# Optimization experiments

Hardware: AMD Instinct MI355X
Metric: run time of the kernel (lower is better)

The kernel has to match this reference:

```python
import jax, jax.numpy as jnp
import numpy as np

EPS = 1e-7
N = 100000
E = 1600000
IN_DIM = 128
OUT_DIM = 128


def _norm(t):
    # clamped L2 norm over last dim, keepdims
    return jnp.clip(jnp.linalg.norm(t, axis=-1, keepdims=True), EPS, None)


def log_map_zero(x, c):
    sqrt_c = jnp.sqrt(c)
    xn = _norm(x)
    y = jnp.clip(sqrt_c * xn, None, 1.0 - 1e-5)
    return jnp.arctanh(y) * x / (sqrt_c * xn)


def exp_map_zero(v, c):
    sqrt_c = jnp.sqrt(c)
    vn = _norm(v)
    return jnp.tanh(sqrt_c * vn) * v / (sqrt_c * vn)


def setup_inputs() -> dict:
    key = jax.random.key(0)
    k1, k2, k3, k4 = jax.random.split(key, 4)
    x = 0.1 * jax.random.normal(k1, (N, IN_DIM), dtype=jnp.float32)  # inside ball
    edge_index = jax.random.randint(k2, (2, E), 0, N, dtype=jnp.int64)
    c = jnp.ones((), dtype=jnp.float32)
    # Xavier-uniform weight (out_dim, in_dim)
    limit = float(np.sqrt(6.0 / (IN_DIM + OUT_DIM)))
    weight = jax.random.uniform(k3, (OUT_DIM, IN_DIM), minval=-limit, maxval=limit, dtype=jnp.float32)
    bias = jnp.zeros((OUT_DIM,), dtype=jnp.float32)
    return {"x": x, "edge_index": edge_index, "c": c, "num_nodes": N,
            "weight": weight, "bias": bias}


def reference(x, edge_index, c, num_nodes, weight, bias):
    # 1. log-map all node features to tangent space at origin
    v = log_map_zero(x, c)  # (N, in_dim)
    src, dst = edge_index[0], edge_index[1]
    # 2. mean aggregation over neighbours (incl. self) via segment_sum
    agg = jax.ops.segment_sum(v[src], dst, num_segments=num_nodes) + v
    count = jax.ops.segment_sum(jnp.ones((src.shape[0],), dtype=v.dtype), dst,
                                num_segments=num_nodes) + 1.0
    v_agg = agg / jnp.clip(count, 1.0, None)[:, None]
    # 3. back to hyperbolic space, then hyperbolic linear
    x_hyp = exp_map_zero(v_agg, c)
    v2 = log_map_zero(x_hyp, c)
    out = v2 @ weight.T + bias
    return exp_map_zero(out, c)
```

## Files before the change

### kernel.cpp

```cpp
#include <hip/hip_runtime.h>
#include <math.h>

#define EPSF 1e-7f
#define YMAXF 0.99999f
#define WPITCH 136

#define NBUCK 256
#define PB_CHUNK 2048

typedef short bf16x8 __attribute__((ext_vector_type(8)));
typedef short bf16x4 __attribute__((ext_vector_type(4)));
typedef float f32x4  __attribute__((ext_vector_type(4)));
typedef int   i32x4  __attribute__((ext_vector_type(4)));

__device__ __forceinline__ float grp32_sum(float v) {
    v += __shfl_xor(v, 1);
    v += __shfl_xor(v, 2);
    v += __shfl_xor(v, 4);
    v += __shfl_xor(v, 8);
    v += __shfl_xor(v, 16);
    return v;
}

__device__ __forceinline__ short f2bf(float f) {
    unsigned u = __float_as_uint(f);
    unsigned r = (u + 0x7FFFu + ((u >> 16) & 1u)) >> 16;
    return (short)r;
}

__device__ __forceinline__ float bf2f(short u) {
    return __uint_as_float(((unsigned)(unsigned short)u) << 16);
}

__device__ __forceinline__ float bf_lo(int w) {
    return __uint_as_float(((unsigned)w) << 16);
}
__device__ __forceinline__ float bf_hi(int w) {
    return __uint_as_float(((unsigned)w) & 0xffff0000u);
}

__global__ void logmap_kernel(const float* __restrict__ x,
                              const float* __restrict__ c_ptr,
                              short* __restrict__ v_bf,
                              int N) {
    int gid = blockIdx.x * blockDim.x + threadIdx.x;
    int row = gid >> 5;
    if (row >= N) return;
    int lane = gid & 31;
    const float4 xv = ((const float4*)x)[(size_t)row * 32 + lane];
    float ss = xv.x * xv.x + xv.y * xv.y + xv.z * xv.z + xv.w * xv.w;
    ss = grp32_sum(ss);
    float sc = sqrtf(c_ptr[0]);
    float xn = fmaxf(sqrtf(ss), EPSF);
    float y = fminf(sc * xn, YMAXF);
    float s = atanhf(y) / (sc * xn);
    bf16x4 pk;
    pk[0] = f2bf(s * xv.x); pk[1] = f2bf(s * xv.y);
    pk[2] = f2bf(s * xv.z); pk[3] = f2bf(s * xv.w);
    *(bf16x4*)&v_bf[(size_t)row * 128 + lane * 4] = pk;
}

__global__ __launch_bounds__(256)
void bucket_count_kernel(const int* __restrict__ eidx_dst,
                         int* __restrict__ bucketCount, int E) {
    __shared__ int h[NBUCK];
    int tid = threadIdx.x;
    h[tid] = 0;
    __syncthreads();
    int per = (E + gridDim.x - 1) / gridDim.x;
    int start = blockIdx.x * per;
    int end = min(start + per, E);
    for (int i = start + tid; i < end; i += 256)
        atomicAdd(&h[eidx_dst[i] >> 9], 1);
    __syncthreads();
    if (h[tid]) atomicAdd(&bucketCount[tid], h[tid]);
}

__global__ __launch_bounds__(256)
void bucket_scan_kernel(const int* __restrict__ bucketCount,
                        int* __restrict__ bucket_base,
                        int* __restrict__ cursor) {
    __shared__ int part[256];
    int tid = threadIdx.x;
    int val = bucketCount[tid];
    part[tid] = val;
    __syncthreads();
    for (int off = 1; off < 256; off <<= 1) {
        int t = (tid >= off) ? part[tid - off] : 0;
        __syncthreads();
        part[tid] += t;
        __syncthreads();
    }
    int excl = part[tid] - val;
    bucket_base[tid] = excl;
    cursor[tid] = excl;
}

__global__ __launch_bounds__(256)
void bucket_scatter_kernel(const int* __restrict__ eidx,
                           int* __restrict__ cursor,
                           int* __restrict__ bucketed, int E) {
    __shared__ int hist[NBUCK];
    __shared__ int lstart[NBUCK];
    __shared__ int gbase[NBUCK];
    __shared__ int part[256];
    __shared__ int stage[PB_CHUNK];
    __shared__ unsigned char stageB[PB_CHUNK];

    int tid = threadIdx.x;
    int start = blockIdx.x * PB_CHUNK;
    int cnt = min(PB_CHUNK, E - start);
    hist[tid] = 0;
    __syncthreads();

    const int J = PB_CHUNK / 256;
    int myP[J], myB[J], myR[J];
    #pragma unroll
    for (int j = 0; j < J; ++j) {
        int idx = j * 256 + tid;
        myR[j] = -1;
        if (idx < cnt) {
            int e = start + idx;
            int d = eidx[E + e];
            int s = eidx[e];
            int b = d >> 9;
            myB[j] = b;
            myP[j] = ((d & 511) << 17) | s;
            myR[j] = atomicAdd(&hist[b], 1);
        }
    }
    __syncthreads();
    part[tid] = hist[tid];
    __syncthreads();
    for (int off = 1; off < 256; off <<= 1) {
        int t = (tid >= off) ? part[tid - off] : 0;
        __syncthreads();
        part[tid] += t;
        __syncthreads();
    }
    lstart[tid] = part[tid] - hist[tid];
    if (hist[tid]) gbase[tid] = atomicAdd(&cursor[tid], hist[tid]);
    __syncthreads();
    #pragma unroll
    for (int j = 0; j < J; ++j) {
        if (myR[j] >= 0) {
            int pos = lstart[myB[j]] + myR[j];
            stage[pos] = myP[j];
            stageB[pos] = (unsigned char)myB[j];
        }
    }
    __syncthreads();
    for (int i = tid; i < cnt; i += 256) {
        int b = stageB[i];
        bucketed[gbase[b] + (i - lstart[b])] = stage[i];
    }
}

__global__ __launch_bounds__(256)
void csr_kernel(const int* __restrict__ bucketed,
                const int* __restrict__ bucket_base,
                const int* __restrict__ cursor_post,
                int* __restrict__ offsets, int* __restrict__ deg,
                int* __restrict__ sorted_src, int N) {
    __shared__ int hist[512];
    __shared__ int pre[512];
    __shared__ int cur[512];
    __shared__ int part[256];
    int b = blockIdx.x;
    int tid = threadIdx.x;
    int start = bucket_base[b];
    int end = cursor_post[b];
    hist[tid] = 0;
    hist[tid + 256] = 0;
    __syncthreads();
    for (int i = start + tid; i < end; i += 256)
        atomicAdd(&hist[bucketed[i] >> 17], 1);
    __syncthreads();
    int a0 = hist[2 * tid], a1 = hist[2 * tid + 1];
    part[tid] = a0 + a1;
    __syncthreads();
    for (int off = 1; off < 256; off <<= 1) {
        int t = (tid >= off) ? part[tid - off] : 0;
        __syncthreads();
        part[tid] += t;
        __syncthreads();
    }
    int base2 = part[tid] - (a0 + a1);
    pre[2 * tid] = base2;
    pre[2 * tid + 1] = base2 + a0;
    cur[2 * tid] = base2;
    cur[2 * tid + 1] = base2 + a0;
    __syncthreads();
    int node0 = b << 9;
    for (int i = tid; i < 512; i += 256) {
        int node = node0 + i;
        if (node < N) { offsets[node] = start + pre[i]; deg[node] = hist[i]; }
    }
    for (int i = start + tid; i < end; i += 256) {
        int p = bucketed[i];
        int ld = p >> 17;
        int src = p & 0x1FFFF;
        int r = atomicAdd(&cur[ld], 1);
        sorted_src[start + r] = src;
    }
}

__global__ __launch_bounds__(256, 3)
void gather_epilogue_kernel(const short* __restrict__ v_bf,
                            const int* __restrict__ sorted_src,
                            const int* __restrict__ offsets,
                            const int* __restrict__ deg,
                            const float* __restrict__ W,
                            const float* __restrict__ bias,
                            const float* __restrict__ c_ptr,
                            float* __restrict__ out,
                            int N) {
    __shared__ short Wl[128 * WPITCH];
    __shared__ short v2l[64 * WPITCH];

    int tid = threadIdx.x;
    for (int i = tid; i < 4096; i += 256) {
        float4 w4 = ((const float4*)W)[i];
        int o = i >> 5;
        int k = (i & 31) * 4;
        bf16x4 w;
        w[0] = f2bf(w4.x); w[1] = f2bf(w4.y); w[2] = f2bf(w4.z); w[3] = f2bf(w4.w);
        *(bf16x4*)&Wl[o * WPITCH + k] = w;
    }

    int wave = tid >> 6;
    int lane = tid & 63;
    int quad = lane >> 4;
    int l16  = lane & 15;
    int g  = tid >> 4;
    int gl = tid & 15;
    float sc = sqrtf(c_ptr[0]);

    float bsv[8];
    #pragma unroll
    for (int c = 0; c < 8; ++c) bsv[c] = bias[c * 16 + l16];

    int row_base = blockIdx.x * 64;

    for (int t = 0; t < 4; ++t) {
        int row = row_base + t * 16 + g;
        bool valid = (row < N);
        float acc[8];
        #pragma unroll
        for (int i = 0; i < 8; ++i) acc[i] = 0.0f;
        int start = 0, d = 0;
        if (valid) {
            start = offsets[row];
            d = deg[row];
            bf16x8 r0 = *(const bf16x8*)&v_bf[(size_t)row * 128 + gl * 8];
            i32x4 w0 = *(const i32x4*)&r0;
            #pragma unroll
            for (int k2 = 0; k2 < 4; ++k2) {
                acc[2 * k2]     = bf_lo(w0[k2]);
                acc[2 * k2 + 1] = bf_hi(w0[k2]);
            }
        }
        for (int j = 0; j < d; j += 16) {
            int m = d - j;
            int batch = sorted_src[start + min(j + gl, d - 1)];

            bf16x8 q0, q1, q2, q3, q4, q5, q6, q7,
                   q8, q9, qA, qB, qC, qD, qE, qF;
#define GLD(i, dst) do {                                                      \
        int src_ = __shfl(batch, (lane & 48) | (i));                          \
        unsigned voff_ = ((unsigned)src_ << 8) | (unsigned)(gl << 4);         \
        asm volatile("global_load_dwordx4 %0, %1, %2"                         \
                     : "=v"(dst) : "v"(voff_), "s"(v_bf));                    \
    } while (0)
            GLD(0, q0);  GLD(1, q1);  GLD(2, q2);  GLD(3, q3);
            GLD(4, q4);  GLD(5, q5);  GLD(6, q6);  GLD(7, q7);
            GLD(8, q8);  GLD(9, q9);  GLD(10, qA); GLD(11, qB);
            GLD(12, qC); GLD(13, qD); GLD(14, qE); GLD(15, qF);
#undef GLD
            asm volatile("s_waitcnt vmcnt(0)" ::: "memory");
            __builtin_amdgcn_sched_barrier(0);

#define ACC(i, rsrc) do {                                                     \
        float w_ = ((i) < m) ? 1.0f : 0.0f;                                   \
        i32x4 wv_ = *(i32x4*)&(rsrc);                                         \
        acc[0] = fmaf(bf_lo(wv_[0]), w_, acc[0]);                             \
        acc[1] = fmaf(bf_hi(wv_[0]), w_, acc[1]);                             \
        acc[2] = fmaf(bf_lo(wv_[1]), w_, acc[2]);                             \
        acc[3] = fmaf(bf_hi(wv_[1]), w_, acc[3]);                             \
        acc[4] = fmaf(bf_lo(wv_[2]), w_, acc[4]);                             \
        acc[5] = fmaf(bf_hi(wv_[2]), w_, acc[5]);                             \
        acc[6] = fmaf(bf_lo(wv_[3]), w_, acc[6]);                             \
        acc[7] = fmaf(bf_hi(wv_[3]), w_, acc[7]);                             \
    } while (0)
            ACC(0, q0);  ACC(1, q1);  ACC(2, q2);  ACC(3, q3);
            ACC(4, q4);  ACC(5, q5);  ACC(6, q6);  ACC(7, q7);
            ACC(8, q8);  ACC(9, q9);  ACC(10, qA); ACC(11, qB);
            ACC(12, qC); ACC(13, qD); ACC(14, qE); ACC(15, qF);
#undef ACC
        }
        float inv = 1.0f / (float)(d + 1);
        #pragma unroll
        for (int i = 0; i < 8; ++i) acc[i] *= inv;

        float ss = 0.0f;
        #pragma unroll
        for (int i = 0; i < 8; ++i) ss += acc[i] * acc[i];
        ss += __shfl_xor(ss, 1);
        ss += __shfl_xor(ss, 2);
        ss += __shfl_xor(ss, 4);
        ss += __shfl_xor(ss, 8);

        float vn  = sqrtf(ss);
        float vnc = fmaxf(vn, EPSF);
        float th  = tanhf(sc * vnc);
        float tt  = th / (sc * vnc);
        float hn  = fmaxf(th / sc, EPSF);
        float y2  = fminf(sc * hn, YMAXF);
        float s2  = atanhf(y2) / (sc * hn);
        float scale = s2 * tt;

        bf16x8 pk;
        #pragma unroll
        for (int i = 0; i < 8; ++i) pk[i] = f2bf(acc[i] * scale);
        *(bf16x8*)&v2l[(t * 16 + g) * WPITCH + gl * 8] = pk;
    }
    __syncthreads();

    f32x4 acc2[8];
    #pragma unroll
    for (int c = 0; c < 8; ++c) acc2[c] = (f32x4){bsv[c], bsv[c], bsv[c], bsv[c]};
    #pragma unroll
    for (int k0 = 0; k0 < 128; k0 += 32) {
        bf16x8 af = *(const bf16x8*)&v2l[(wave * 16 + l16) * WPITCH + k0 + quad * 8];
        #pragma unroll
        for (int c = 0; c < 8; ++c) {
            bf16x8 bf = *(const bf16x8*)&Wl[(c * 16 + l16) * WPITCH + k0 + quad * 8];
            acc2[c] = __builtin_amdgcn_mfma_f32_16x16x32_bf16(af, bf, acc2[c], 0, 0, 0);
        }
    }

    #pragma unroll
    for (int r = 0; r < 4; ++r) {
        float ss = 0.0f;
        #pragma unroll
        for (int c = 0; c < 8; ++c) ss += acc2[c][r] * acc2[c][r];
        ss += __shfl_xor(ss, 1);
        ss += __shfl_xor(ss, 2);
        ss += __shfl_xor(ss, 4);
        ss += __shfl_xor(ss, 8);
        float on  = sqrtf(ss);
        float onc = fmaxf(on, EPSF);
        float gsc = tanhf(sc * onc) / (sc * onc);
        int orow = row_base + wave * 16 + quad * 4 + r;
        if (orow < N) {
            size_t base = (size_t)orow * 128;
            #pragma unroll
            for (int c = 0; c < 8; ++c)
                out[base + c * 16 + l16] = gsc * acc2[c][r];
        }
    }
}

extern "C" void kernel_launch(void* const* d_in, const int* in_sizes, int n_in,
                              void* d_out, int out_size, void* d_ws, size_t ws_size,
                              hipStream_t stream) {
    const float* x     = (const float*)d_in[0];
    const int*   eidx  = (const int*)d_in[1];
    const float* c_ptr = (const float*)d_in[2];
    const float* W     = (const float*)d_in[4];
    const float* bias  = (const float*)d_in[5];
    float* out = (float*)d_out;

    int N = in_sizes[0] / 128;
    int E = in_sizes[1] / 2;

    short* v_bf        = (short*)d_ws;
    int*   deg         = (int*)(v_bf + (size_t)N * 128);
    int*   offsets     = deg + N;
    int*   bucketCount = offsets + N;
    int*   bucket_base = bucketCount + NBUCK;
    int*   cursor      = bucket_base + NBUCK;
    int*   bucketed    = cursor + NBUCK;
    int*   sorted_src  = bucketed + E;

    hipMemsetAsync(bucketCount, 0, NBUCK * sizeof(int), stream);

    {
        long long threads = (long long)N * 32;
        int blocks = (int)((threads + 255) / 256);
        hipLaunchKernelGGL(logmap_kernel, dim3(blocks), dim3(256), 0, stream,
                           x, c_ptr, v_bf, N);
    }
    hipLaunchKernelGGL(bucket_count_kernel, dim3(256), dim3(256), 0, stream,
                       eidx + E, bucketCount, E);
    hipLaunchKernelGGL(bucket_scan_kernel, dim3(1), dim3(256), 0, stream,
                       bucketCount, bucket_base, cursor);
    {
        int blocks = (E + PB_CHUNK - 1) / PB_CHUNK;
        hipLaunchKernelGGL(bucket_scatter_kernel, dim3(blocks), dim3(256), 0, stream,
                           eidx, cursor, bucketed, E);
    }
    {
        int blocks = (N + 511) / 512;
        hipLaunchKernelGGL(csr_kernel, dim3(blocks), dim3(256), 0, stream,
                           bucketed, bucket_base, cursor, offsets, deg, sorted_src, N);
    }
    {
        int blocks = (N + 63) / 64;
        hipLaunchKernelGGL(gather_epilogue_kernel, dim3(blocks), dim3(256), 0, stream,
                           v_bf, sorted_src, offsets, deg, W, bias, c_ptr, out, N);
    }
}
```

Measured before the change: 266.8 us.

## Precompute bf16 weights once, drop LDS weight tile, prefetch neighbor indices

The fp32→bf16 weight conversion and the bucket-count zeroing move into the logmap kernel, replacing the per-block LDS weight staging and the separate memset. The gather kernel now reads weight fragments straight from global/L2, which frees LDS so occupancy can rise (launch bounds 3→4 blocks). It also preloads offsets and degrees for all four row tiles, prefetches the next batch of neighbor indices, and splits the load wait so the first half of accumulation overlaps the remaining loads. The cost is that MFMA B operands now come from global memory rather than LDS, which may add latency in the epilogue.

```diff
diff --git a/kernel.cpp b/kernel.cpp
--- a/kernel.cpp
+++ b/kernel.cpp
@@ -28,10 +28,6 @@
     return (short)r;
 }
 
-__device__ __forceinline__ float bf2f(short u) {
-    return __uint_as_float(((unsigned)(unsigned short)u) << 16);
-}
-
 __device__ __forceinline__ float bf_lo(int w) {
     return __uint_as_float(((unsigned)w) << 16);
 }
@@ -39,11 +35,22 @@
     return __uint_as_float(((unsigned)w) & 0xffff0000u);
 }
 
-__global__ void logmap_kernel(const float* __restrict__ x,
-                              const float* __restrict__ c_ptr,
-                              short* __restrict__ v_bf,
-                              int N) {
+__global__ __launch_bounds__(256)
+void logmap_kernel(const float* __restrict__ x,
+                   const float* __restrict__ c_ptr,
+                   short* __restrict__ v_bf,
+                   const float* __restrict__ W,
+                   short* __restrict__ W_bf,
+                   int* __restrict__ bucketCount,
+                   int N) {
     int gid = blockIdx.x * blockDim.x + threadIdx.x;
+    if (gid < NBUCK) bucketCount[gid] = 0;
+    if (gid < 4096) {
+        float4 w4 = ((const float4*)W)[gid];
+        bf16x4 w;
+        w[0] = f2bf(w4.x); w[1] = f2bf(w4.y); w[2] = f2bf(w4.z); w[3] = f2bf(w4.w);
+        *(bf16x4*)&W_bf[gid * 4] = w;
+    }
     int row = gid >> 5;
     if (row >= N) return;
     int lane = gid & 31;
@@ -205,29 +212,19 @@
     }
 }
 
-__global__ __launch_bounds__(256, 3)
+__global__ __launch_bounds__(256, 4)
 void gather_epilogue_kernel(const short* __restrict__ v_bf,
                             const int* __restrict__ sorted_src,
                             const int* __restrict__ offsets,
                             const int* __restrict__ deg,
-                            const float* __restrict__ W,
+                            const short* __restrict__ W_bf,
                             const float* __restrict__ bias,
                             const float* __restrict__ c_ptr,
                             float* __restrict__ out,
                             int N) {
-    __shared__ short Wl[128 * WPITCH];
     __shared__ short v2l[64 * WPITCH];
 
     int tid = threadIdx.x;
-    for (int i = tid; i < 4096; i += 256) {
-        float4 w4 = ((const float4*)W)[i];
-        int o = i >> 5;
-        int k = (i & 31) * 4;
-        bf16x4 w;
-        w[0] = f2bf(w4.x); w[1] = f2bf(w4.y); w[2] = f2bf(w4.z); w[3] = f2bf(w4.w);
-        *(bf16x4*)&Wl[o * WPITCH + k] = w;
-    }
-
     int wave = tid >> 6;
     int lane = tid & 63;
     int quad = lane >> 4;
@@ -242,16 +239,23 @@
 
     int row_base = blockIdx.x * 64;
 
+    int offs[4], degs[4];
+    #pragma unroll
+    for (int t = 0; t < 4; ++t) {
+        int row = row_base + t * 16 + g;
+        bool valid = (row < N);
+        offs[t] = valid ? offsets[row] : 0;
+        degs[t] = valid ? deg[row] : 0;
+    }
+
     for (int t = 0; t < 4; ++t) {
         int row = row_base + t * 16 + g;
         bool valid = (row < N);
         float acc[8];
         #pragma unroll
         for (int i = 0; i < 8; ++i) acc[i] = 0.0f;
-        int start = 0, d = 0;
+        int start = offs[t], d = degs[t];
         if (valid) {
-            start = offsets[row];
-            d = deg[row];
             bf16x8 r0 = *(const bf16x8*)&v_bf[(size_t)row * 128 + gl * 8];
             i32x4 w0 = *(const i32x4*)&r0;
             #pragma unroll
@@ -260,12 +264,14 @@
                 acc[2 * k2 + 1] = bf_hi(w0[k2]);
             }
         }
+        int batch = (d > 0) ? sorted_src[start + min(gl, d - 1)] : 0;
         for (int j = 0; j < d; j += 16) {
             int m = d - j;
-            int batch = sorted_src[start + min(j + gl, d - 1)];
+            int nb = (j + 16 < d) ? sorted_src[start + min(j + 16 + gl, d - 1)] : 0;
 
             bf16x8 q0, q1, q2, q3, q4, q5, q6, q7,
                    q8, q9, qA, qB, qC, qD, qE, qF;
+            __builtin_amdgcn_sched_barrier(0);
 #define GLD(i, dst) do {                                                      \
         int src_ = __shfl(batch, (lane & 48) | (i));                          \
         unsigned voff_ = ((unsigned)src_ << 8) | (unsigned)(gl << 4);         \
@@ -277,7 +283,7 @@
             GLD(8, q8);  GLD(9, q9);  GLD(10, qA); GLD(11, qB);
             GLD(12, qC); GLD(13, qD); GLD(14, qE); GLD(15, qF);
 #undef GLD
-            asm volatile("s_waitcnt vmcnt(0)" ::: "memory");
+            asm volatile("s_waitcnt vmcnt(8)" ::: "memory");
             __builtin_amdgcn_sched_barrier(0);
 
 #define ACC(i, rsrc) do {                                                     \
@@ -294,9 +300,12 @@
     } while (0)
             ACC(0, q0);  ACC(1, q1);  ACC(2, q2);  ACC(3, q3);
             ACC(4, q4);  ACC(5, q5);  ACC(6, q6);  ACC(7, q7);
+            asm volatile("s_waitcnt vmcnt(0)" ::: "memory");
+            __builtin_amdgcn_sched_barrier(0);
             ACC(8, q8);  ACC(9, q9);  ACC(10, qA); ACC(11, qB);
             ACC(12, qC); ACC(13, qD); ACC(14, qE); ACC(15, qF);
 #undef ACC
+            batch = nb;
         }
         float inv = 1.0f / (float)(d + 1);
         #pragma unroll
@@ -334,8 +343,8 @@
         bf16x8 af = *(const bf16x8*)&v2l[(wave * 16 + l16) * WPITCH + k0 + quad * 8];
         #pragma unroll
         for (int c = 0; c < 8; ++c) {
-            bf16x8 bf = *(const bf16x8*)&Wl[(c * 16 + l16) * WPITCH + k0 + quad * 8];
-            acc2[c] = __builtin_amdgcn_mfma_f32_16x16x32_bf16(af, bf, acc2[c], 0, 0, 0);
+            bf16x8 bw = *(const bf16x8*)&W_bf[(c * 16 + l16) * 128 + k0 + quad * 8];
+            acc2[c] = __builtin_amdgcn_mfma_f32_16x16x32_bf16(af, bw, acc2[c], 0, 0, 0);
         }
     }
 
@@ -380,16 +389,15 @@
     int*   bucketCount = offsets + N;
     int*   bucket_base = bucketCount + NBUCK;
     int*   cursor      = bucket_base + NBUCK;
-    int*   bucketed    = cursor + NBUCK;
+    short* W_bf        = (short*)(cursor + NBUCK);
+    int*   bucketed    = (int*)(W_bf + 128 * 128);
     int*   sorted_src  = bucketed + E;
-
-    hipMemsetAsync(bucketCount, 0, NBUCK * sizeof(int), stream);
 
     {
         long long threads = (long long)N * 32;
         int blocks = (int)((threads + 255) / 256);
         hipLaunchKernelGGL(logmap_kernel, dim3(blocks), dim3(256), 0, stream,
-                           x, c_ptr, v_bf, N);
+                           x, c_ptr, v_bf, W, W_bf, bucketCount, N);
     }
     hipLaunchKernelGGL(bucket_count_kernel, dim3(256), dim3(256), 0, stream,
                        eidx + E, bucketCount, E);
@@ -408,6 +416,6 @@
     {
         int blocks = (N + 63) / 64;
         hipLaunchKernelGGL(gather_epilogue_kernel, dim3(blocks), dim3(256), 0, stream,
-                           v_bf, sorted_src, offsets, deg, W, bias, c_ptr, out, N);
-    }
-}
+                           v_bf, sorted_src, offsets, deg, W_bf, bias, c_ptr, out, N);
+    }
+}
```

Measured after the change: 271.5 us. Within noise of the previous version (+1.8%).
